# Optimization experiments

Measured on AMD Instinct MI355X. Metric: run time of the kernel, lower is better.

Reference implementation:

```python
import jax, jax.numpy as jnp
import numpy as np

B = 2048
NUM_ITER = 3  # dynamic routing iterations


def _conv2d(x, w, b, pad):
    # x: [B,C,H,W], w: [O,I,kh,kw] (OIHW)
    y = jax.lax.conv_general_dilated(
        x, w, window_strides=(1, 1), padding=[(pad, pad), (pad, pad)],
        dimension_numbers=('NCHW', 'OIHW', 'NCHW'))
    return y + b[None, :, None, None]


def _maxpool2(x):
    return jax.lax.reduce_window(x, -jnp.inf, jax.lax.max,
                                 (1, 1, 2, 2), (1, 1, 2, 2), 'VALID')


def _squash(t, axis=-1):
    # scale = |t|^2/(1+|t|^2); out = scale * t / |t|
    n2 = jnp.sum(t * t, axis=axis, keepdims=True)
    return (n2 / (1.0 + n2)) * t * jax.lax.rsqrt(n2)


def setup_inputs() -> dict:
    key = jax.random.key(0)
    ks = jax.random.split(key, 8)
    f32 = jnp.float32
    rn = lambda k, s, sc=1.0: jax.random.normal(k, s, f32) * sc
    return {
        'x': rn(ks[0], (B, 1, 36, 60)),
        'y': rn(ks[1], (B, 2)),
        'conv1_w': rn(ks[2], (20, 1, 5, 5), 0.1),
        'conv1_b': jnp.zeros((20,), f32),
        'conv2_w': rn(ks[3], (50, 20, 5, 5), 0.01),
        'conv2_b': jnp.zeros((50,), f32),
        'pcaps_w': rn(ks[4], (16, 50, 5, 5), 0.05),   # 4 capsules x 4 out-ch, stacked
        'pcaps_b': jnp.zeros((16,), f32),
        'route_w': rn(ks[5], (2, 288, 4, 1)),          # [num_caps, route_nodes, in_ch, out_ch]
        'fc1_w': rn(ks[6], (500, 3602), 0.02),
        'fc1_b': jnp.zeros((500,), f32),
        'fc2_w': rn(ks[7], (2, 502), 0.05),
        'fc2_b': jnp.zeros((2,), f32),
    }


def reference(x, y, conv1_w, conv1_b, conv2_w, conv2_b, pcaps_w, pcaps_b,
              route_w, fc1_w, fc1_b, fc2_w, fc2_b):
    b = x.shape[0]
    # conv backbone
    h = _maxpool2(_conv2d(x, conv1_w, conv1_b, 0))   # [B,20,16,28]
    h = _maxpool2(_conv2d(h, conv2_w, conv2_b, 0))   # [B,50,6,12]

    # primary capsules: 4 parallel convs (stacked into one), each [B,4,6,12]
    p = _conv2d(h, pcaps_w, pcaps_b, 2)              # [B,16,6,12]
    u = p.reshape(b, 4, 4 * 6 * 12)                  # [B, caps=4, nodes=288] (c,h,w flatten per capsule)
    u = u.transpose(0, 2, 1)                         # [B,288,4]
    u = _squash(u, axis=-1)

    # digit capsules: dynamic routing
    # priors[k,b,r,o] = sum_c u[b,r,c] * W[k,r,c,o]
    priors = jnp.einsum('brc,krco->kbro', u, route_w)  # [2,B,288,1]
    logits = jnp.zeros_like(priors)
    v = None
    for i in range(NUM_ITER):
        probs = jax.nn.softmax(logits, axis=2)
        v = _squash(jnp.sum(probs * priors, axis=2, keepdims=True), axis=-1)  # [2,B,1,1]
        if i < NUM_ITER - 1:
            logits = logits + jnp.sum(priors * v, axis=-1, keepdims=True)

    c = v[:, :, 0, :].transpose(1, 0, 2).reshape(b, -1)  # [B,2]
    xf = h.reshape(b, -1)                                # [B,3600]
    f = jnp.concatenate([xf, c], axis=-1)                # [B,3602]
    f = jax.nn.relu(f @ fc1_w.T + fc1_b)                 # [B,500]
    f = jnp.concatenate([f, y], axis=1)                  # [B,502]
    return f @ fc2_w.T + fc2_b                           # [B,2]
```

## Files before the change

kernel.cpp:

```cpp
#include <hip/hip_runtime.h>
#include <math.h>


#define BATCH 2048

typedef __attribute__((ext_vector_type(8))) short short8;
typedef __attribute__((ext_vector_type(4))) float floatx4;
typedef unsigned short u16;
typedef unsigned int   u32;

__device__ inline float wave_sum(float v) {
#pragma unroll
    for (int off = 32; off >= 1; off >>= 1) v += __shfl_xor(v, off);
    return v;
}
__device__ inline float wave_max(float v) {
#pragma unroll
    for (int off = 32; off >= 1; off >>= 1) v = fmaxf(v, __shfl_xor(v, off));
    return v;
}
__device__ inline u16 f2bf(float f) {
    u32 u = __float_as_uint(f);
    u32 r = (u + 0x7FFFu + ((u >> 16) & 1u)) >> 16;
    return (u16)r;
}

__global__ __launch_bounds__(256) void k_prep(
    const float* __restrict__ fw,  u16* __restrict__ w_bf,
    const float* __restrict__ w2,  u16* __restrict__ w2t,
    const float* __restrict__ pcw, u16* __restrict__ w_pc,
    const float* __restrict__ w1,  u16* __restrict__ w1t,
    const float* __restrict__ y,   const float* __restrict__ f2w,
    const float* __restrict__ f2b, float* __restrict__ out)
{
    __shared__ __align__(16) float srow[3600];
    const int blk = blockIdx.x, t = threadIdx.x;
    if (blk < 500) {
        const int n = blk;
        const float* src = fw + (size_t)n * 3602;
        for (int i = t; i < 1800; i += 256)
            *(float2*)&srow[2 * i] = *(const float2*)&src[2 * i];
        __syncthreads();
        u32* dst = (u32*)(w_bf + (size_t)n * 3616);
        for (int i = t; i < 1808; i += 256) {
            int k2 = 2 * i;
            u32 pk = 0u;
            if (k2 < 3600) {
                int pos = k2 / 50, oc = k2 - 50 * pos;
                pk = (u32)f2bf(srow[oc * 72 + pos])
                   | ((u32)f2bf(srow[(oc + 1) * 72 + pos]) << 16);
            }
            dst[i] = pk;
        }
    } else if (blk == 500) {
        u32* z = (u32*)(w_bf + (size_t)500 * 3616);
        for (int i = t; i < 21696; i += 256) z[i] = 0u;
    } else if (blk < 526) {
        int g   = (blk - 501) * 256 + t;
        int idx = g * 8;
        int tap = idx >> 11;
        int oc  = (idx >> 5) & 63;
        int ic0 = idx & 31;
        u16 v[8];
#pragma unroll
        for (int j = 0; j < 8; ++j) {
            int ic = ic0 + j;
            float f = (ic < 20 && oc < 50) ? w2[oc * 500 + ic * 25 + tap] : 0.f;
            v[j] = f2bf(f);
        }
        *(short8*)&w2t[idx] = *(short8*)v;
    } else if (blk < 539) {
        int g = (blk - 526) * 256 + t;
        if (g >= 3200) return;
        int idx = g * 8;
        int tap = idx >> 10;
        int rem = idx & 1023;
        int oc  = rem >> 6;
        int ic0 = rem & 63;
        u16 v[8];
#pragma unroll
        for (int j = 0; j < 8; ++j) {
            int ic = ic0 + j;
            float f = (ic < 50) ? pcw[(oc * 50 + ic) * 25 + tap] : 0.f;
            v[j] = f2bf(f);
        }
        *(short8*)&w_pc[idx] = *(short8*)v;
    } else if (blk == 539) {
        if (t < 128) {
            int n  = t >> 2;
            int k0 = (t & 3) * 8;
            u16 v[8];
#pragma unroll
            for (int j = 0; j < 8; ++j) {
                int k = k0 + j;
                float f = (n < 20 && k < 25) ? w1[n * 25 + k] : 0.f;
                v[j] = f2bf(f);
            }
            *(short8*)&w1t[t * 8] = *(short8*)v;
        }
    } else {
        int b = (blk - 540) * 256 + t;
        float y0 = y[b * 2], y1 = y[b * 2 + 1];
        float2 o;
        o.x = f2b[0] + y0 * f2w[500] + y1 * f2w[501];
        o.y = f2b[1] + y0 * f2w[502 + 500] + y1 * f2w[502 + 501];
        *(float2*)&out[b * 2] = o;
    }
}

__global__ __launch_bounds__(256, 3) void k_convs(
    const float* __restrict__ x, const u16* __restrict__ w1t,
    const float* __restrict__ b1, const u16* __restrict__ w2t,
    const float* __restrict__ b2, const u16* __restrict__ w_pc,
    const float* __restrict__ pcb, const float* __restrict__ rw,
    u32* __restrict__ h_bf, float* __restrict__ cbuf)
{
    __shared__ __align__(16) u16 smem[24704];
    u16* h1t = smem;
    u16* xbf = smem + 17920;
    u16* im2 = smem + 20224;

    const int t = threadIdx.x;
    const int b = blockIdx.x;

    for (int i = t; i < 2688; i += 256) {
        int pos = i / 6, c = i - 6 * pos;
        ((u32*)h1t)[pos * 20 + 10 + c] = 0u;
    }
    const float* xb = x + b * 2160;
    for (int i = t; i < 2160; i += 256) {
        int r = i / 60, c = i - 60 * r;
        xbf[r * 64 + c] = f2bf(xb[i]);
    }
    __syncthreads();

    const int lane = t & 63, w = t >> 6;
    const int r16  = lane & 15;
    const int q    = lane >> 4;

    short8 w1f[2];
#pragma unroll
    for (int nt = 0; nt < 2; ++nt)
        w1f[nt] = *(const short8*)&w1t[(nt * 16 + r16) * 32 + q * 8];

    const int p_   = t;
    const int px_  = p_ >> 2;
    const int dy_  = (p_ & 3) >> 1, dx_ = p_ & 1;
    const int xc_  = 2 * px_ + dx_;
    const int j0_  = xc_ >> 1;
    const int par_ = xc_ & 1;

#pragma unroll 1
    for (int c = 0; c < 16; ++c) {
        if (t < 112) {
            u16 tap[25];
#pragma unroll
            for (int r = 0; r < 5; ++r) {
                const u32* U = (const u32*)&xbf[(2 * c + dy_ + r) * 64];
                u32 A0 = U[j0_], A1 = U[j0_ + 1], A2 = U[j0_ + 2];
                u16 e0 = par_ ? (u16)(A0 >> 16) : (u16)A0;
                u16 e1 = par_ ? (u16)A1         : (u16)(A0 >> 16);
                u16 e2 = par_ ? (u16)(A1 >> 16) : (u16)A1;
                u16 e3 = par_ ? (u16)A2         : (u16)(A1 >> 16);
                u16 e4 = par_ ? (u16)(A2 >> 16) : (u16)A2;
                tap[r * 5 + 0] = e0; tap[r * 5 + 1] = e1; tap[r * 5 + 2] = e2;
                tap[r * 5 + 3] = e3; tap[r * 5 + 4] = e4;
            }
            u32 ow[16];
#pragma unroll
            for (int j = 0; j < 12; ++j)
                ow[j] = (u32)tap[2 * j] | ((u32)tap[2 * j + 1] << 16);
            ow[12] = (u32)tap[24];
            ow[13] = 0u; ow[14] = 0u; ow[15] = 0u;
            u32* dst = (u32*)&im2[p_ * 40];
            *(uint4*)&dst[0]  = make_uint4(ow[0],  ow[1],  ow[2],  ow[3]);
            *(uint4*)&dst[4]  = make_uint4(ow[4],  ow[5],  ow[6],  ow[7]);
            *(uint4*)&dst[8]  = make_uint4(ow[8],  ow[9],  ow[10], ow[11]);
            *(uint4*)&dst[12] = make_uint4(ow[12], ow[13], ow[14], ow[15]);
        }
        __syncthreads();
#pragma unroll
        for (int mi = 0; mi < 2; ++mi) {
            int mt = w + 4 * mi;
            if (mt < 7) {
                short8 af = *(const short8*)&im2[(mt * 16 + r16) * 40 + q * 8];
                floatx4 a1[2] = {};
#pragma unroll
                for (int nt = 0; nt < 2; ++nt)
                    a1[nt] = __builtin_amdgcn_mfma_f32_16x16x32_bf16(
                        af, w1f[nt], a1[nt], 0, 0, 0);
                int pq = mt * 4 + q;
#pragma unroll
                for (int nt = 0; nt < 2; ++nt) {
                    int oc = nt * 16 + r16;
                    if (oc < 20) {
                        floatx4 a = a1[nt];
                        float v = fmaxf(fmaxf(a[0], a[1]), fmaxf(a[2], a[3]))
                                + b1[oc];
                        h1t[(c * 28 + pq) * 40 + oc] = f2bf(v);
                    }
                }
            }
        }
        __syncthreads();
    }

    int abase[5];
#pragma unroll
    for (int i = 0; i < 5; ++i) {
        int mt = w + 4 * i;
        if (mt < 18) {
            int m  = mt * 16 + r16;
            int pq = m >> 2, sub = m & 3;
            int py = pq / 12, px = pq - py * 12;
            int yy = py * 2 + (sub >> 1);
            int xx = px * 2 + (sub & 1);
            abase[i] = (yy * 28 + xx) * 40 + q * 8;
        } else abase[i] = 0;
    }
    floatx4 acc2[5][4] = {};
    const u16* wtb = w2t + r16 * 32 + q * 8;

    short8 bf[4];
#pragma unroll
    for (int nt = 0; nt < 4; ++nt)
        bf[nt] = *(const short8*)&wtb[nt * 512];

#pragma unroll 1
    for (int tap = 0; tap < 25; ++tap) {
        short8 bfn[4];
        if (tap < 24) {
#pragma unroll
            for (int nt = 0; nt < 4; ++nt)
                bfn[nt] = *(const short8*)&wtb[(tap + 1) * 2048 + nt * 512];
        }
        int r = tap / 5, s = tap - 5 * r;
        int aoff = r * 1120 + s * 40;
#pragma unroll
        for (int i = 0; i < 5; ++i) {
            int mt = w + 4 * i;
            if (mt < 18) {
                short8 af = *(const short8*)&h1t[abase[i] + aoff];
#pragma unroll
                for (int nt = 0; nt < 4; ++nt)
                    acc2[i][nt] = __builtin_amdgcn_mfma_f32_16x16x32_bf16(
                        af, bf[nt], acc2[i][nt], 0, 0, 0);
            }
        }
#pragma unroll
        for (int nt = 0; nt < 4; ++nt) bf[nt] = bfn[nt];
    }
    __syncthreads();

    float* hs2 = (float*)smem;
#pragma unroll
    for (int i = 0; i < 5; ++i) {
        int mt = w + 4 * i;
        if (mt < 18) {
            int pq = mt * 4 + q;
#pragma unroll
            for (int nt = 0; nt < 4; ++nt) {
                int oc = nt * 16 + r16;
                if (oc < 50) {
                    floatx4 a = acc2[i][nt];
                    float v = fmaxf(fmaxf(a[0], a[1]), fmaxf(a[2], a[3])) + b2[oc];
                    hs2[pq * 50 + oc] = v;
                }
            }
        }
    }
    for (int i = t; i < 6336; i += 256)
        ((u32*)smem)[3600 + i] = 0u;
    __syncthreads();

    u16* hsbuf = smem + 7200;
    u32* ho = h_bf + (size_t)b * 1808;
    for (int i = t; i < 1808; i += 256) {
        if (i < 1800) {
            int k2 = 2 * i;
            u32 pk = (u32)f2bf(hs2[k2]) | ((u32)f2bf(hs2[k2 + 1]) << 16);
            ho[i] = pk;
            int pos = k2 / 50;
            int oc  = k2 - 50 * pos;
            int ph  = pos / 12, pw = pos - 12 * ph;
            ((u32*)hsbuf)[((((ph + 2) * 16) + pw + 2) * 72 + oc) >> 1] = pk;
        } else ho[i] = 0u;
    }
    __syncthreads();

    int pbase[5];
#pragma unroll
    for (int mt = 0; mt < 5; ++mt) {
        int m  = mt * 16 + r16;
        int ph = m / 12, pw = m - 12 * ph;
        pbase[mt] = (ph * 16 + pw) * 72 + q * 8;
    }
    floatx4 pacc[5] = {};
    const u16* wp = w_pc + r16 * 64 + q * 8;
    const int ntap = (28 - w) >> 2;
#pragma unroll 1
    for (int tt = 0; tt < ntap; ++tt) {
        int tap = w + 4 * tt;
        short8 b0 = *(const short8*)&wp[tap * 1024];
        short8 b1 = *(const short8*)&wp[tap * 1024 + 32];
        int r = tap / 5, s = tap - 5 * r;
        int aoff = (r * 16 + s) * 72;
#pragma unroll
        for (int mt = 0; mt < 5; ++mt) {
            short8 a0 = *(const short8*)&hsbuf[pbase[mt] + aoff];
            short8 a1 = *(const short8*)&hsbuf[pbase[mt] + aoff + 32];
            pacc[mt] = __builtin_amdgcn_mfma_f32_16x16x32_bf16(a0, b0, pacc[mt], 0, 0, 0);
            pacc[mt] = __builtin_amdgcn_mfma_f32_16x16x32_bf16(a1, b1, pacc[mt], 0, 0, 0);
        }
    }
    __syncthreads();

    float* psum = (float*)(smem + 7200);
#pragma unroll
    for (int mt = 0; mt < 5; ++mt)
#pragma unroll
        for (int i = 0; i < 4; ++i) {
            int m = mt * 16 + q * 4 + i;
            psum[w * 1280 + m * 16 + r16] = pacc[mt][i];
        }
    __syncthreads();

    for (int i = t; i < 1152; i += 256) {
        float s = psum[i] + psum[1280 + i] + psum[2560 + i] + psum[3840 + i]
                + pcb[i & 15];
        psum[i] = s;
    }
    __syncthreads();

    float* pri = (float*)(smem + 19872);
    for (int r = t; r < 288; r += 256) {
        int sub = r / 72;
        int pos = r - sub * 72;
        float u0 = psum[pos * 16 + 0  + sub];
        float u1 = psum[pos * 16 + 4  + sub];
        float u2 = psum[pos * 16 + 8  + sub];
        float u3 = psum[pos * 16 + 12 + sub];
        float n2 = u0 * u0 + u1 * u1 + u2 * u2 + u3 * u3;
        float scale = (n2 / (1.0f + n2)) * rsqrtf(n2);
        u0 *= scale; u1 *= scale; u2 *= scale; u3 *= scale;
#pragma unroll
        for (int k = 0; k < 2; ++k) {
            const float4 wv = *(const float4*)&rw[(k * 288 + r) * 4];
            pri[k * 288 + r] = u0 * wv.x + u1 * wv.y + u2 * wv.z + u3 * wv.w;
        }
    }
    __syncthreads();

    if (w < 2) {
        const float* pr = &pri[w * 288];
        float p[5];
        bool  val[5];
#pragma unroll
        for (int j = 0; j < 5; ++j) {
            int r  = j * 64 + lane;
            val[j] = r < 288;
            p[j]   = val[j] ? pr[r] : 0.0f;
        }
        float tot = wave_sum(p[0] + p[1] + p[2] + p[3] + p[4]);
        float s = tot * (1.0f / 288.0f);
        float a = s * fabsf(s) / (1.0f + s * s);
#pragma unroll
        for (int it = 0; it < 2; ++it) {
            float l[5];
            float lm = -INFINITY;
#pragma unroll
            for (int j = 0; j < 5; ++j) {
                l[j] = val[j] ? p[j] * a : -INFINITY;
                lm   = fmaxf(lm, l[j]);
            }
            lm = wave_max(lm);
            float se = 0.f, sp = 0.f;
#pragma unroll
            for (int j = 0; j < 5; ++j) {
                float e = val[j] ? expf(l[j] - lm) : 0.f;
                se += e;
                sp += e * p[j];
            }
            se = wave_sum(se);
            sp = wave_sum(sp);
            float sv = sp / se;
            float v  = sv * fabsf(sv) / (1.0f + sv * sv);
            if (it == 0) a += v;
            else if (lane == 0) cbuf[b * 2 + w] = v;
        }
    }
}

__global__ __launch_bounds__(256) void k_fc1(
    const u16* __restrict__ h_bf, const u16* __restrict__ w_bf,
    const float* __restrict__ cc, const float* __restrict__ w,
    const float* __restrict__ bias, const float* __restrict__ f2w,
    float* __restrict__ out)
{
    __shared__ __align__(16) u16 As[64 * 40];
    __shared__ __align__(16) u16 Bs[64 * 40];
    const int t  = threadIdx.x;
    const int m0 = blockIdx.x * 64;
    const int n0 = blockIdx.y * 64;
    const int row = t >> 2, c8 = (t & 3) * 8;
    const u16* ha = &h_bf[(size_t)(m0 + row) * 3616 + c8];
    const u16* wa = &w_bf[(size_t)(n0 + row) * 3616 + c8];
    short8 areg = *(const short8*)ha;
    short8 breg = *(const short8*)wa;
    const int lane = t & 63, wv = t >> 6;
    const int r16 = lane & 15, q = lane >> 4;
    const int wr = row * 40 + (t & 3) * 8;
    const int ar = (wv * 16 + r16) * 40 + q * 8;
    const int br = r16 * 40 + q * 8;
    floatx4 acc[4] = {};
#pragma unroll 1
    for (int it = 0; it < 113; ++it) {
        __syncthreads();
        *(short8*)&As[wr] = areg;
        *(short8*)&Bs[wr] = breg;
        __syncthreads();
        if (it < 112) {
            areg = *(const short8*)(ha + (it + 1) * 32);
            breg = *(const short8*)(wa + (it + 1) * 32);
        }
        short8 af = *(const short8*)&As[ar];
#pragma unroll
        for (int nt = 0; nt < 4; ++nt) {
            short8 bfv = *(const short8*)&Bs[nt * 640 + br];
            acc[nt] = __builtin_amdgcn_mfma_f32_16x16x32_bf16(af, bfv, acc[nt], 0, 0, 0);
        }
    }
    const int mbase = m0 + wv * 16 + q * 4;
    float s0[4] = {0.f, 0.f, 0.f, 0.f};
    float s1[4] = {0.f, 0.f, 0.f, 0.f};
#pragma unroll
    for (int nt = 0; nt < 4; ++nt) {
        int n = n0 + nt * 16 + r16;
        if (n < 500) {
            float bn  = bias[n];
            float wc0 = w[(size_t)n * 3602 + 3600];
            float wc1 = w[(size_t)n * 3602 + 3601];
            float w20 = f2w[n];
            float w21 = f2w[502 + n];
#pragma unroll
            for (int i = 0; i < 4; ++i) {
                int m = mbase + i;
                float v = fmaxf(acc[nt][i] + bn + cc[m * 2] * wc0
                                + cc[m * 2 + 1] * wc1, 0.f);
                s0[i] += v * w20;
                s1[i] += v * w21;
            }
        }
    }
#pragma unroll
    for (int i = 0; i < 4; ++i) {
        float a0 = s0[i], a1 = s1[i];
#pragma unroll
        for (int off = 1; off <= 8; off <<= 1) {
            a0 += __shfl_xor(a0, off);
            a1 += __shfl_xor(a1, off);
        }
        if (r16 == 0) {
            int m = mbase + i;
            atomicAdd(&out[m * 2], a0);
            atomicAdd(&out[m * 2 + 1], a1);
        }
    }
}

extern "C" void kernel_launch(void* const* d_in, const int* in_sizes, int n_in,
                              void* d_out, int out_size, void* d_ws, size_t ws_size,
                              hipStream_t stream) {
    const float* x    = (const float*)d_in[0];
    const float* y    = (const float*)d_in[1];
    const float* c1w  = (const float*)d_in[2];
    const float* c1b  = (const float*)d_in[3];
    const float* c2w  = (const float*)d_in[4];
    const float* c2b  = (const float*)d_in[5];
    const float* pcw  = (const float*)d_in[6];
    const float* pcb  = (const float*)d_in[7];
    const float* rw   = (const float*)d_in[8];
    const float* f1w  = (const float*)d_in[9];
    const float* f1b  = (const float*)d_in[10];
    const float* f2w  = (const float*)d_in[11];
    const float* f2b  = (const float*)d_in[12];
    float* out = (float*)d_out;

    u32*   h_bf = (u32*)d_ws;
    u16*   w_bf = (u16*)(h_bf + (size_t)BATCH * 1808);
    u16*   w2t  = w_bf + (size_t)512 * 3616;
    u16*   w_pc = w2t + 51200;
    u16*   w1t  = w_pc + 25600;
    float* cbuf = (float*)(w1t + 1024);

    k_prep<<<548, 256, 0, stream>>>(f1w, w_bf, c2w, w2t, pcw, w_pc, c1w, w1t,
                                    y, f2w, f2b, out);
    k_convs<<<BATCH, 256, 0, stream>>>(x, w1t, c1b, w2t, c2b, w_pc, pcb, rw,
                                       h_bf, cbuf);
    dim3 g4(32, 8);
    k_fc1<<<g4, 256, 0, stream>>>((const u16*)h_bf, w_bf, cbuf, f1w, f1b,
                                  f2w, out);
}
```

Baseline: 259.1 us.

## Build conv1 MFMA operands directly in registers, split conv2 accumulators, double-buffer fc1

Conv1 no longer stages an im2col tile in shared memory. Each lane now assembles its bf16 MFMA A-fragment straight from the input rows in registers, which removes the im2col buffer and the per-row barriers. Conv2 is split into two passes (3 tiles, then 2) to cut live accumulators, and the kernel asks for 4 blocks per CU instead of 3. fc1 moves to 32-row M tiles with double-buffered LDS and one barrier per step, doubling the grid. The cost is more register-side shuffling and redundant B-weight loads across the two conv2 passes.

```diff
diff --git a/kernel.cpp b/kernel.cpp
--- a/kernel.cpp
+++ b/kernel.cpp
@@ -23,6 +23,12 @@
     u32 u = __float_as_uint(f);
     u32 r = (u + 0x7FFFu + ((u >> 16) & 1u)) >> 16;
     return (u16)r;
+}
+__device__ inline void ext5(short8 v, int par, u16 e[5]) {
+    union { short8 s; u16 a[8]; } u; u.s = v;
+#pragma unroll
+    for (int s5 = 0; s5 < 5; ++s5)
+        e[s5] = par ? u.a[s5 + 1] : u.a[s5];
 }
 
 __global__ __launch_bounds__(256) void k_prep(
@@ -108,17 +114,16 @@
     }
 }
 
-__global__ __launch_bounds__(256, 3) void k_convs(
+__global__ __launch_bounds__(256, 4) void k_convs(
     const float* __restrict__ x, const u16* __restrict__ w1t,
     const float* __restrict__ b1, const u16* __restrict__ w2t,
     const float* __restrict__ b2, const u16* __restrict__ w_pc,
     const float* __restrict__ pcb, const float* __restrict__ rw,
     u32* __restrict__ h_bf, float* __restrict__ cbuf)
 {
-    __shared__ __align__(16) u16 smem[24704];
+    __shared__ __align__(16) u16 smem[20224];
     u16* h1t = smem;
     u16* xbf = smem + 17920;
-    u16* im2 = smem + 20224;
 
     const int t = threadIdx.x;
     const int b = blockIdx.x;
@@ -143,132 +148,181 @@
     for (int nt = 0; nt < 2; ++nt)
         w1f[nt] = *(const short8*)&w1t[(nt * 16 + r16) * 32 + q * 8];
 
-    const int p_   = t;
-    const int px_  = p_ >> 2;
-    const int dy_  = (p_ & 3) >> 1, dx_ = p_ & 1;
-    const int xc_  = 2 * px_ + dx_;
-    const int j0_  = xc_ >> 1;
-    const int par_ = xc_ & 1;
-
 #pragma unroll 1
-    for (int c = 0; c < 16; ++c) {
-        if (t < 112) {
-            u16 tap[25];
-#pragma unroll
-            for (int r = 0; r < 5; ++r) {
-                const u32* U = (const u32*)&xbf[(2 * c + dy_ + r) * 64];
-                u32 A0 = U[j0_], A1 = U[j0_ + 1], A2 = U[j0_ + 2];
-                u16 e0 = par_ ? (u16)(A0 >> 16) : (u16)A0;
-                u16 e1 = par_ ? (u16)A1         : (u16)(A0 >> 16);
-                u16 e2 = par_ ? (u16)(A1 >> 16) : (u16)A1;
-                u16 e3 = par_ ? (u16)A2         : (u16)(A1 >> 16);
-                u16 e4 = par_ ? (u16)(A2 >> 16) : (u16)A2;
-                tap[r * 5 + 0] = e0; tap[r * 5 + 1] = e1; tap[r * 5 + 2] = e2;
-                tap[r * 5 + 3] = e3; tap[r * 5 + 4] = e4;
-            }
-            u32 ow[16];
-#pragma unroll
-            for (int j = 0; j < 12; ++j)
-                ow[j] = (u32)tap[2 * j] | ((u32)tap[2 * j + 1] << 16);
-            ow[12] = (u32)tap[24];
-            ow[13] = 0u; ow[14] = 0u; ow[15] = 0u;
-            u32* dst = (u32*)&im2[p_ * 40];
-            *(uint4*)&dst[0]  = make_uint4(ow[0],  ow[1],  ow[2],  ow[3]);
-            *(uint4*)&dst[4]  = make_uint4(ow[4],  ow[5],  ow[6],  ow[7]);
-            *(uint4*)&dst[8]  = make_uint4(ow[8],  ow[9],  ow[10], ow[11]);
-            *(uint4*)&dst[12] = make_uint4(ow[12], ow[13], ow[14], ow[15]);
+    for (int jj = 0; jj < 28; ++jj) {
+        int jb = w + 4 * jj;
+        int mt = jb % 7;
+        int c  = jb / 7;
+        int p  = mt * 16 + r16;
+        int px = p >> 2;
+        int dy = (p >> 1) & 1, dx = p & 1;
+        int xc = 2 * px + dx;
+        int par = xc & 1;
+        int rowbase = (2 * c + dy) * 64 + (xc & ~1);
+        union { short8 s; u16 a[8]; } af;
+        if (q == 0) {
+            short8 vA = *(const short8*)&xbf[rowbase];
+            short8 vB = *(const short8*)&xbf[rowbase + 64];
+            u16 eA[5], eB[5];
+            ext5(vA, par, eA); ext5(vB, par, eB);
+            af.a[0]=eA[0]; af.a[1]=eA[1]; af.a[2]=eA[2]; af.a[3]=eA[3];
+            af.a[4]=eA[4]; af.a[5]=eB[0]; af.a[6]=eB[1]; af.a[7]=eB[2];
+        } else if (q == 1) {
+            short8 vB = *(const short8*)&xbf[rowbase + 64];
+            short8 vC = *(const short8*)&xbf[rowbase + 128];
+            short8 vD = *(const short8*)&xbf[rowbase + 192];
+            u16 eB[5], eC[5], eD[5];
+            ext5(vB, par, eB); ext5(vC, par, eC); ext5(vD, par, eD);
+            af.a[0]=eB[3]; af.a[1]=eB[4]; af.a[2]=eC[0]; af.a[3]=eC[1];
+            af.a[4]=eC[2]; af.a[5]=eC[3]; af.a[6]=eC[4]; af.a[7]=eD[0];
+        } else if (q == 2) {
+            short8 vD = *(const short8*)&xbf[rowbase + 192];
+            short8 vE = *(const short8*)&xbf[rowbase + 256];
+            u16 eD[5], eE[5];
+            ext5(vD, par, eD); ext5(vE, par, eE);
+            af.a[0]=eD[1]; af.a[1]=eD[2]; af.a[2]=eD[3]; af.a[3]=eD[4];
+            af.a[4]=eE[0]; af.a[5]=eE[1]; af.a[6]=eE[2]; af.a[7]=eE[3];
+        } else {
+            short8 vE = *(const short8*)&xbf[rowbase + 256];
+            u16 eE[5];
+            ext5(vE, par, eE);
+            af.a[0]=eE[4];
+#pragma unroll
+            for (int j = 1; j < 8; ++j) af.a[j] = 0;
+        }
+        floatx4 a1[2] = {};
+#pragma unroll
+        for (int nt = 0; nt < 2; ++nt)
+            a1[nt] = __builtin_amdgcn_mfma_f32_16x16x32_bf16(
+                af.s, w1f[nt], a1[nt], 0, 0, 0);
+        int pq = mt * 4 + q;
+#pragma unroll
+        for (int nt = 0; nt < 2; ++nt) {
+            int oc = nt * 16 + r16;
+            if (oc < 20) {
+                floatx4 a = a1[nt];
+                float v = fmaxf(fmaxf(a[0], a[1]), fmaxf(a[2], a[3])) + b1[oc];
+                h1t[(c * 28 + pq) * 40 + oc] = f2bf(v);
+            }
+        }
+    }
+    __syncthreads();
+
+    const u16* wtb = w2t + r16 * 32 + q * 8;
+    float* hs2 = (float*)smem;
+
+    {
+        int abase[3];
+#pragma unroll
+        for (int i = 0; i < 3; ++i) {
+            int m  = (w + 4 * i) * 16 + r16;
+            int pq = m >> 2, sub = m & 3;
+            int py = pq / 12, px2 = pq - py * 12;
+            int yy = py * 2 + (sub >> 1);
+            int xx = px2 * 2 + (sub & 1);
+            abase[i] = (yy * 28 + xx) * 40 + q * 8;
+        }
+        floatx4 acc[3][4] = {};
+        short8 bf[4];
+#pragma unroll
+        for (int nt = 0; nt < 4; ++nt)
+            bf[nt] = *(const short8*)&wtb[nt * 512];
+#pragma unroll 1
+        for (int tap = 0; tap < 25; ++tap) {
+            short8 bfn[4];
+            if (tap < 24) {
+#pragma unroll
+                for (int nt = 0; nt < 4; ++nt)
+                    bfn[nt] = *(const short8*)&wtb[(tap + 1) * 2048 + nt * 512];
+            }
+            int r = tap / 5, s = tap - 5 * r;
+            int aoff = r * 1120 + s * 40;
+#pragma unroll
+            for (int i = 0; i < 3; ++i) {
+                short8 af = *(const short8*)&h1t[abase[i] + aoff];
+#pragma unroll
+                for (int nt = 0; nt < 4; ++nt)
+                    acc[i][nt] = __builtin_amdgcn_mfma_f32_16x16x32_bf16(
+                        af, bf[nt], acc[i][nt], 0, 0, 0);
+            }
+#pragma unroll
+            for (int nt = 0; nt < 4; ++nt) bf[nt] = bfn[nt];
         }
         __syncthreads();
 #pragma unroll
-        for (int mi = 0; mi < 2; ++mi) {
-            int mt = w + 4 * mi;
-            if (mt < 7) {
-                short8 af = *(const short8*)&im2[(mt * 16 + r16) * 40 + q * 8];
-                floatx4 a1[2] = {};
-#pragma unroll
-                for (int nt = 0; nt < 2; ++nt)
-                    a1[nt] = __builtin_amdgcn_mfma_f32_16x16x32_bf16(
-                        af, w1f[nt], a1[nt], 0, 0, 0);
-                int pq = mt * 4 + q;
-#pragma unroll
-                for (int nt = 0; nt < 2; ++nt) {
-                    int oc = nt * 16 + r16;
-                    if (oc < 20) {
-                        floatx4 a = a1[nt];
-                        float v = fmaxf(fmaxf(a[0], a[1]), fmaxf(a[2], a[3]))
-                                + b1[oc];
-                        h1t[(c * 28 + pq) * 40 + oc] = f2bf(v);
-                    }
-                }
-            }
-        }
-        __syncthreads();
-    }
-
-    int abase[5];
-#pragma unroll
-    for (int i = 0; i < 5; ++i) {
-        int mt = w + 4 * i;
-        if (mt < 18) {
-            int m  = mt * 16 + r16;
-            int pq = m >> 2, sub = m & 3;
-            int py = pq / 12, px = pq - py * 12;
-            int yy = py * 2 + (sub >> 1);
-            int xx = px * 2 + (sub & 1);
-            abase[i] = (yy * 28 + xx) * 40 + q * 8;
-        } else abase[i] = 0;
-    }
-    floatx4 acc2[5][4] = {};
-    const u16* wtb = w2t + r16 * 32 + q * 8;
-
-    short8 bf[4];
-#pragma unroll
-    for (int nt = 0; nt < 4; ++nt)
-        bf[nt] = *(const short8*)&wtb[nt * 512];
-
-#pragma unroll 1
-    for (int tap = 0; tap < 25; ++tap) {
-        short8 bfn[4];
-        if (tap < 24) {
-#pragma unroll
-            for (int nt = 0; nt < 4; ++nt)
-                bfn[nt] = *(const short8*)&wtb[(tap + 1) * 2048 + nt * 512];
-        }
-        int r = tap / 5, s = tap - 5 * r;
-        int aoff = r * 1120 + s * 40;
-#pragma unroll
-        for (int i = 0; i < 5; ++i) {
-            int mt = w + 4 * i;
-            if (mt < 18) {
-                short8 af = *(const short8*)&h1t[abase[i] + aoff];
-#pragma unroll
-                for (int nt = 0; nt < 4; ++nt)
-                    acc2[i][nt] = __builtin_amdgcn_mfma_f32_16x16x32_bf16(
-                        af, bf[nt], acc2[i][nt], 0, 0, 0);
-            }
-        }
-#pragma unroll
-        for (int nt = 0; nt < 4; ++nt) bf[nt] = bfn[nt];
-    }
-    __syncthreads();
-
-    float* hs2 = (float*)smem;
-#pragma unroll
-    for (int i = 0; i < 5; ++i) {
-        int mt = w + 4 * i;
-        if (mt < 18) {
-            int pq = mt * 4 + q;
+        for (int i = 0; i < 3; ++i) {
+            int pq = (w + 4 * i) * 4 + q;
 #pragma unroll
             for (int nt = 0; nt < 4; ++nt) {
                 int oc = nt * 16 + r16;
                 if (oc < 50) {
-                    floatx4 a = acc2[i][nt];
-                    float v = fmaxf(fmaxf(a[0], a[1]), fmaxf(a[2], a[3])) + b2[oc];
-                    hs2[pq * 50 + oc] = v;
+                    floatx4 a = acc[i][nt];
+                    hs2[pq * 50 + oc] =
+                        fmaxf(fmaxf(a[0], a[1]), fmaxf(a[2], a[3])) + b2[oc];
                 }
             }
         }
     }
+    {
+        int abase[2];
+        bool vld[2];
+#pragma unroll
+        for (int i = 0; i < 2; ++i) {
+            int mt = w + 12 + 4 * i;
+            vld[i] = (mt < 18);
+            int m  = (vld[i] ? mt : 12) * 16 + r16;
+            int pq = m >> 2, sub = m & 3;
+            int py = pq / 12, px2 = pq - py * 12;
+            int yy = py * 2 + (sub >> 1);
+            int xx = px2 * 2 + (sub & 1);
+            abase[i] = (yy * 28 + xx) * 40 + q * 8;
+        }
+        floatx4 acc[2][4] = {};
+        short8 bf[4];
+#pragma unroll
+        for (int nt = 0; nt < 4; ++nt)
+            bf[nt] = *(const short8*)&wtb[nt * 512];
+#pragma unroll 1
+        for (int tap = 0; tap < 25; ++tap) {
+            short8 bfn[4];
+            if (tap < 24) {
+#pragma unroll
+                for (int nt = 0; nt < 4; ++nt)
+                    bfn[nt] = *(const short8*)&wtb[(tap + 1) * 2048 + nt * 512];
+            }
+            int r = tap / 5, s = tap - 5 * r;
+            int aoff = r * 1120 + s * 40;
+#pragma unroll
+            for (int i = 0; i < 2; ++i) {
+                if (vld[i]) {
+                    short8 af = *(const short8*)&h1t[abase[i] + aoff];
+#pragma unroll
+                    for (int nt = 0; nt < 4; ++nt)
+                        acc[i][nt] = __builtin_amdgcn_mfma_f32_16x16x32_bf16(
+                            af, bf[nt], acc[i][nt], 0, 0, 0);
+                }
+            }
+#pragma unroll
+            for (int nt = 0; nt < 4; ++nt) bf[nt] = bfn[nt];
+        }
+#pragma unroll
+        for (int i = 0; i < 2; ++i) {
+            if (vld[i]) {
+                int pq = (w + 12 + 4 * i) * 4 + q;
+#pragma unroll
+                for (int nt = 0; nt < 4; ++nt) {
+                    int oc = nt * 16 + r16;
+                    if (oc < 50) {
+                        floatx4 a = acc[i][nt];
+                        hs2[pq * 50 + oc] =
+                            fmaxf(fmaxf(a[0], a[1]), fmaxf(a[2], a[3])) + b2[oc];
+                    }
+                }
+            }
+        }
+    }
+    __syncthreads();
+
     for (int i = t; i < 6336; i += 256)
         ((u32*)smem)[3600 + i] = 0u;
     __syncthreads();
@@ -332,7 +386,7 @@
     }
     __syncthreads();
 
-    float* pri = (float*)(smem + 19872);
+    float* pri = (float*)(smem + 17440);
     for (int r = t; r < 288; r += 256) {
         int sub = r / 72;
         int pos = r - sub * 72;
@@ -397,45 +451,50 @@
     const float* __restrict__ bias, const float* __restrict__ f2w,
     float* __restrict__ out)
 {
-    __shared__ __align__(16) u16 As[64 * 40];
-    __shared__ __align__(16) u16 Bs[64 * 40];
+    __shared__ __align__(16) u16 As[2][32 * 40];
+    __shared__ __align__(16) u16 Bs[2][64 * 40];
     const int t  = threadIdx.x;
-    const int m0 = blockIdx.x * 64;
+    const int m0 = blockIdx.x * 32;
     const int n0 = blockIdx.y * 64;
-    const int row = t >> 2, c8 = (t & 3) * 8;
-    const u16* ha = &h_bf[(size_t)(m0 + row) * 3616 + c8];
-    const u16* wa = &w_bf[(size_t)(n0 + row) * 3616 + c8];
-    short8 areg = *(const short8*)ha;
-    short8 breg = *(const short8*)wa;
     const int lane = t & 63, wv = t >> 6;
     const int r16 = lane & 15, q = lane >> 4;
-    const int wr = row * 40 + (t & 3) * 8;
-    const int ar = (wv * 16 + r16) * 40 + q * 8;
-    const int br = r16 * 40 + q * 8;
-    floatx4 acc[4] = {};
+    const int row = t >> 2, c8 = (t & 3) * 8;
+    const bool aload = (t < 128);
+    const u16* ha = &h_bf[(size_t)(m0 + (row & 31)) * 3616 + c8];
+    const u16* wa = &w_bf[(size_t)(n0 + row) * 3616 + c8];
+    short8 areg = {};
+    if (aload) areg = *(const short8*)ha;
+    short8 breg = *(const short8*)wa;
+    const int mt  = wv & 1;
+    const int ntb = (wv >> 1) * 2;
+    const int awr = (row & 31) * 40 + c8;
+    const int bwr = row * 40 + c8;
+    const int ar  = (mt * 16 + r16) * 40 + q * 8;
+    const int br0 = (ntb * 16 + r16) * 40 + q * 8;
+    floatx4 acc[2] = {};
 #pragma unroll 1
     for (int it = 0; it < 113; ++it) {
+        const int buf = it & 1;
+        if (aload) *(short8*)&As[buf][awr] = areg;
+        *(short8*)&Bs[buf][bwr] = breg;
+        if (it < 112) {
+            if (aload) areg = *(const short8*)(ha + (it + 1) * 32);
+            breg = *(const short8*)(wa + (it + 1) * 32);
+        }
         __syncthreads();
-        *(short8*)&As[wr] = areg;
-        *(short8*)&Bs[wr] = breg;
-        __syncthreads();
-        if (it < 112) {
-            areg = *(const short8*)(ha + (it + 1) * 32);
-            breg = *(const short8*)(wa + (it + 1) * 32);
-        }
-        short8 af = *(const short8*)&As[ar];
-#pragma unroll
-        for (int nt = 0; nt < 4; ++nt) {
-            short8 bfv = *(const short8*)&Bs[nt * 640 + br];
-            acc[nt] = __builtin_amdgcn_mfma_f32_16x16x32_bf16(af, bfv, acc[nt], 0, 0, 0);
-        }
-    }
-    const int mbase = m0 + wv * 16 + q * 4;
+        short8 af = *(const short8*)&As[buf][ar];
+#pragma unroll
+        for (int jn = 0; jn < 2; ++jn) {
+            short8 bfv = *(const short8*)&Bs[buf][br0 + jn * 640];
+            acc[jn] = __builtin_amdgcn_mfma_f32_16x16x32_bf16(af, bfv, acc[jn], 0, 0, 0);
+        }
+    }
+    const int mbase = m0 + mt * 16 + q * 4;
     float s0[4] = {0.f, 0.f, 0.f, 0.f};
     float s1[4] = {0.f, 0.f, 0.f, 0.f};
 #pragma unroll
-    for (int nt = 0; nt < 4; ++nt) {
-        int n = n0 + nt * 16 + r16;
+    for (int jn = 0; jn < 2; ++jn) {
+        int n = n0 + (ntb + jn) * 16 + r16;
         if (n < 500) {
             float bn  = bias[n];
             float wc0 = w[(size_t)n * 3602 + 3600];
@@ -445,7 +504,7 @@
 #pragma unroll
             for (int i = 0; i < 4; ++i) {
                 int m = mbase + i;
-                float v = fmaxf(acc[nt][i] + bn + cc[m * 2] * wc0
+                float v = fmaxf(acc[jn][i] + bn + cc[m * 2] * wc0
                                 + cc[m * 2 + 1] * wc1, 0.f);
                 s0[i] += v * w20;
                 s1[i] += v * w21;
@@ -497,7 +556,7 @@
                                     y, f2w, f2b, out);
     k_convs<<<BATCH, 256, 0, stream>>>(x, w1t, c1b, w2t, c2b, w_pc, pcb, rw,
                                        h_bf, cbuf);
-    dim3 g4(32, 8);
+    dim3 g4(64, 8);
     k_fc1<<<g4, 256, 0, stream>>>((const u16*)h_bf, w_bf, cbuf, f1w, f1b,
                                   f2w, out);
 }
```

Result: slower. 283.5 us (+9.4%).

## Double-buffer fc1 LDS tiles and double the K step per iteration

Applied to the files above, without the earlier changes.

The fc1 GEMM kernel now keeps two LDS buffers and loads a 64-wide K slice per iteration instead of 32. This cuts the barriers to one per iteration and halves the iteration count. The padded K stride grows from 3616 to 3648 so it is a multiple of 64, which means updating the weight prep, the activation writes and the workspace offsets to match. In exchange the kernel uses more LDS and more registers for the prefetch, and the extra zero padding adds a little memory traffic.

```diff
diff --git a/kernel.cpp b/kernel.cpp
--- a/kernel.cpp
+++ b/kernel.cpp
@@ -3,6 +3,7 @@
 
 
 #define BATCH 2048
+#define KP 3648
 
 typedef __attribute__((ext_vector_type(8))) short short8;
 typedef __attribute__((ext_vector_type(4))) float floatx4;
@@ -41,8 +42,8 @@
         for (int i = t; i < 1800; i += 256)
             *(float2*)&srow[2 * i] = *(const float2*)&src[2 * i];
         __syncthreads();
-        u32* dst = (u32*)(w_bf + (size_t)n * 3616);
-        for (int i = t; i < 1808; i += 256) {
+        u32* dst = (u32*)(w_bf + (size_t)n * KP);
+        for (int i = t; i < 1824; i += 256) {
             int k2 = 2 * i;
             u32 pk = 0u;
             if (k2 < 3600) {
@@ -53,8 +54,8 @@
             dst[i] = pk;
         }
     } else if (blk == 500) {
-        u32* z = (u32*)(w_bf + (size_t)500 * 3616);
-        for (int i = t; i < 21696; i += 256) z[i] = 0u;
+        u32* z = (u32*)(w_bf + (size_t)500 * KP);
+        for (int i = t; i < 21888; i += 256) z[i] = 0u;
     } else if (blk < 526) {
         int g   = (blk - 501) * 256 + t;
         int idx = g * 8;
@@ -263,8 +264,8 @@
                 int oc = nt * 16 + r16;
                 if (oc < 50) {
                     floatx4 a = acc2[i][nt];
-                    float v = fmaxf(fmaxf(a[0], a[1]), fmaxf(a[2], a[3])) + b2[oc];
-                    hs2[pq * 50 + oc] = v;
+                    hs2[pq * 50 + oc] =
+                        fmaxf(fmaxf(a[0], a[1]), fmaxf(a[2], a[3])) + b2[oc];
                 }
             }
         }
@@ -274,8 +275,8 @@
     __syncthreads();
 
     u16* hsbuf = smem + 7200;
-    u32* ho = h_bf + (size_t)b * 1808;
-    for (int i = t; i < 1808; i += 256) {
+    u32* ho = h_bf + (size_t)b * 1824;
+    for (int i = t; i < 1824; i += 256) {
         if (i < 1800) {
             int k2 = 2 * i;
             u32 pk = (u32)f2bf(hs2[k2]) | ((u32)f2bf(hs2[k2 + 1]) << 16);
@@ -397,37 +398,49 @@
     const float* __restrict__ bias, const float* __restrict__ f2w,
     float* __restrict__ out)
 {
-    __shared__ __align__(16) u16 As[64 * 40];
-    __shared__ __align__(16) u16 Bs[64 * 40];
+    __shared__ __align__(16) u16 As[2][64 * 72];
+    __shared__ __align__(16) u16 Bs[2][64 * 72];
     const int t  = threadIdx.x;
     const int m0 = blockIdx.x * 64;
     const int n0 = blockIdx.y * 64;
-    const int row = t >> 2, c8 = (t & 3) * 8;
-    const u16* ha = &h_bf[(size_t)(m0 + row) * 3616 + c8];
-    const u16* wa = &w_bf[(size_t)(n0 + row) * 3616 + c8];
-    short8 areg = *(const short8*)ha;
-    short8 breg = *(const short8*)wa;
+    const int row = t >> 2, seg = t & 3;
+    const u16* ha = &h_bf[(size_t)(m0 + row) * KP + seg * 16];
+    const u16* wa = &w_bf[(size_t)(n0 + row) * KP + seg * 16];
+    short8 a0 = *(const short8*)ha;
+    short8 a1 = *(const short8*)(ha + 8);
+    short8 b0 = *(const short8*)wa;
+    short8 b1 = *(const short8*)(wa + 8);
     const int lane = t & 63, wv = t >> 6;
     const int r16 = lane & 15, q = lane >> 4;
-    const int wr = row * 40 + (t & 3) * 8;
-    const int ar = (wv * 16 + r16) * 40 + q * 8;
-    const int br = r16 * 40 + q * 8;
+    const int wr = row * 72 + seg * 16;
+    const int ar = (wv * 16 + r16) * 72 + q * 8;
+    const int br = r16 * 72 + q * 8;
     floatx4 acc[4] = {};
 #pragma unroll 1
-    for (int it = 0; it < 113; ++it) {
+    for (int it = 0; it < 57; ++it) {
+        const int buf = it & 1;
+        *(short8*)&As[buf][wr]     = a0;
+        *(short8*)&As[buf][wr + 8] = a1;
+        *(short8*)&Bs[buf][wr]     = b0;
+        *(short8*)&Bs[buf][wr + 8] = b1;
+        if (it < 56) {
+            const u16* han = ha + (it + 1) * 64;
+            const u16* wan = wa + (it + 1) * 64;
+            a0 = *(const short8*)han;
+            a1 = *(const short8*)(han + 8);
+            b0 = *(const short8*)wan;
+            b1 = *(const short8*)(wan + 8);
+        }
         __syncthreads();
-        *(short8*)&As[wr] = areg;
-        *(short8*)&Bs[wr] = breg;
-        __syncthreads();
-        if (it < 112) {
-            areg = *(const short8*)(ha + (it + 1) * 32);
-            breg = *(const short8*)(wa + (it + 1) * 32);
-        }
-        short8 af = *(const short8*)&As[ar];
-#pragma unroll
-        for (int nt = 0; nt < 4; ++nt) {
-            short8 bfv = *(const short8*)&Bs[nt * 640 + br];
-            acc[nt] = __builtin_amdgcn_mfma_f32_16x16x32_bf16(af, bfv, acc[nt], 0, 0, 0);
+#pragma unroll
+        for (int s = 0; s < 2; ++s) {
+            short8 af = *(const short8*)&As[buf][ar + s * 32];
+#pragma unroll
+            for (int nt = 0; nt < 4; ++nt) {
+                short8 bfv = *(const short8*)&Bs[buf][br + nt * 1152 + s * 32];
+                acc[nt] = __builtin_amdgcn_mfma_f32_16x16x32_bf16(
+                    af, bfv, acc[nt], 0, 0, 0);
+            }
         }
     }
     const int mbase = m0 + wv * 16 + q * 4;
@@ -454,16 +467,16 @@
     }
 #pragma unroll
     for (int i = 0; i < 4; ++i) {
-        float a0 = s0[i], a1 = s1[i];
+        float a0r = s0[i], a1r = s1[i];
 #pragma unroll
         for (int off = 1; off <= 8; off <<= 1) {
-            a0 += __shfl_xor(a0, off);
-            a1 += __shfl_xor(a1, off);
+            a0r += __shfl_xor(a0r, off);
+            a1r += __shfl_xor(a1r, off);
         }
         if (r16 == 0) {
             int m = mbase + i;
-            atomicAdd(&out[m * 2], a0);
-            atomicAdd(&out[m * 2 + 1], a1);
+            atomicAdd(&out[m * 2], a0r);
+            atomicAdd(&out[m * 2 + 1], a1r);
         }
     }
 }
@@ -487,8 +500,8 @@
     float* out = (float*)d_out;
 
     u32*   h_bf = (u32*)d_ws;
-    u16*   w_bf = (u16*)(h_bf + (size_t)BATCH * 1808);
-    u16*   w2t  = w_bf + (size_t)512 * 3616;
+    u16*   w_bf = (u16*)(h_bf + (size_t)BATCH * 1824);
+    u16*   w2t  = w_bf + (size_t)512 * KP;
     u16*   w_pc = w2t + 51200;
     u16*   w1t  = w_pc + 25600;
     float* cbuf = (float*)(w1t + 1024);
```

New measurement: 237.2 us. 8.4% less time.

## Split-K FC1 with global_load_lds tiles and separate FC2 reduction kernel

Applied to the files above, without the earlier changes.

The FC1 GEMM is restructured into a split-K kernel (4 K-slices, 128x64 tiles) that loads tiles directly into LDS via global_load_lds, and writes partial sums to a workspace. A new k_fc2 kernel then sums the partials, applies bias, capsule terms and ReLU, and computes the FC2 outputs without atomics, using a precomputed per-neuron weight table. K padding grows to 3712 to divide evenly, and the psum LDS layout is padded to stride 17 to avoid bank conflicts. This aims to raise parallelism and memory throughput in FC1, at the cost of an extra launch and a large fp32 partial-sum buffer round trip.

```diff
diff --git a/kernel.cpp b/kernel.cpp
--- a/kernel.cpp
+++ b/kernel.cpp
@@ -3,11 +3,16 @@
 
 
 #define BATCH 2048
+#define KP 3712
 
 typedef __attribute__((ext_vector_type(8))) short short8;
 typedef __attribute__((ext_vector_type(4))) float floatx4;
 typedef unsigned short u16;
 typedef unsigned int   u32;
+
+#define GLD(gp, lp) __builtin_amdgcn_global_load_lds( \
+    (const __attribute__((address_space(1))) u32*)(gp), \
+    (__attribute__((address_space(3))) u32*)(lp), 16, 0, 0)
 
 __device__ inline float wave_sum(float v) {
 #pragma unroll
@@ -30,8 +35,8 @@
     const float* __restrict__ w2,  u16* __restrict__ w2t,
     const float* __restrict__ pcw, u16* __restrict__ w_pc,
     const float* __restrict__ w1,  u16* __restrict__ w1t,
-    const float* __restrict__ y,   const float* __restrict__ f2w,
-    const float* __restrict__ f2b, float* __restrict__ out)
+    const float* __restrict__ f1b, const float* __restrict__ f2w,
+    float* __restrict__ wtab)
 {
     __shared__ __align__(16) float srow[3600];
     const int blk = blockIdx.x, t = threadIdx.x;
@@ -41,8 +46,8 @@
         for (int i = t; i < 1800; i += 256)
             *(float2*)&srow[2 * i] = *(const float2*)&src[2 * i];
         __syncthreads();
-        u32* dst = (u32*)(w_bf + (size_t)n * 3616);
-        for (int i = t; i < 1808; i += 256) {
+        u32* dst = (u32*)(w_bf + (size_t)n * KP);
+        for (int i = t; i < 1856; i += 256) {
             int k2 = 2 * i;
             u32 pk = 0u;
             if (k2 < 3600) {
@@ -53,8 +58,8 @@
             dst[i] = pk;
         }
     } else if (blk == 500) {
-        u32* z = (u32*)(w_bf + (size_t)500 * 3616);
-        for (int i = t; i < 21696; i += 256) z[i] = 0u;
+        u32* z = (u32*)(w_bf + (size_t)500 * KP);
+        for (int i = t; i < 22272; i += 256) z[i] = 0u;
     } else if (blk < 526) {
         int g   = (blk - 501) * 256 + t;
         int idx = g * 8;
@@ -99,12 +104,18 @@
             *(short8*)&w1t[t * 8] = *(short8*)v;
         }
     } else {
-        int b = (blk - 540) * 256 + t;
-        float y0 = y[b * 2], y1 = y[b * 2 + 1];
-        float2 o;
-        o.x = f2b[0] + y0 * f2w[500] + y1 * f2w[501];
-        o.y = f2b[1] + y0 * f2w[502 + 500] + y1 * f2w[502 + 501];
-        *(float2*)&out[b * 2] = o;
+        for (int nn = t; nn < 512; nn += 256) {
+            float bias = 0.f, wc0 = 0.f, wc1 = 0.f, f20 = 0.f, f21 = 0.f;
+            if (nn < 500) {
+                bias = f1b[nn];
+                wc0  = fw[(size_t)nn * 3602 + 3600];
+                wc1  = fw[(size_t)nn * 3602 + 3601];
+                f20  = f2w[nn];
+                f21  = f2w[502 + nn];
+            }
+            *(float4*)&wtab[nn * 8]     = make_float4(bias, wc0, wc1, f20);
+            *(float4*)&wtab[nn * 8 + 4] = make_float4(f21, 0.f, 0.f, 0.f);
+        }
     }
 }
 
@@ -263,8 +274,8 @@
                 int oc = nt * 16 + r16;
                 if (oc < 50) {
                     floatx4 a = acc2[i][nt];
-                    float v = fmaxf(fmaxf(a[0], a[1]), fmaxf(a[2], a[3])) + b2[oc];
-                    hs2[pq * 50 + oc] = v;
+                    hs2[pq * 50 + oc] =
+                        fmaxf(fmaxf(a[0], a[1]), fmaxf(a[2], a[3])) + b2[oc];
                 }
             }
         }
@@ -274,8 +285,8 @@
     __syncthreads();
 
     u16* hsbuf = smem + 7200;
-    u32* ho = h_bf + (size_t)b * 1808;
-    for (int i = t; i < 1808; i += 256) {
+    u32* ho = h_bf + (size_t)b * 1856;
+    for (int i = t; i < 1856; i += 256) {
         if (i < 1800) {
             int k2 = 2 * i;
             u32 pk = (u32)f2bf(hs2[k2]) | ((u32)f2bf(hs2[k2 + 1]) << 16);
@@ -321,14 +332,16 @@
 #pragma unroll
         for (int i = 0; i < 4; ++i) {
             int m = mt * 16 + q * 4 + i;
-            psum[w * 1280 + m * 16 + r16] = pacc[mt][i];
+            psum[w * 1360 + m * 17 + r16] = pacc[mt][i];
         }
     __syncthreads();
 
     for (int i = t; i < 1152; i += 256) {
-        float s = psum[i] + psum[1280 + i] + psum[2560 + i] + psum[3840 + i]
-                + pcb[i & 15];
-        psum[i] = s;
+        int m = i >> 4, oc = i & 15;
+        int a = m * 17 + oc;
+        float s = psum[a] + psum[1360 + a] + psum[2720 + a] + psum[4080 + a]
+                + pcb[oc];
+        psum[a] = s;
     }
     __syncthreads();
 
@@ -336,10 +349,10 @@
     for (int r = t; r < 288; r += 256) {
         int sub = r / 72;
         int pos = r - sub * 72;
-        float u0 = psum[pos * 16 + 0  + sub];
-        float u1 = psum[pos * 16 + 4  + sub];
-        float u2 = psum[pos * 16 + 8  + sub];
-        float u3 = psum[pos * 16 + 12 + sub];
+        float u0 = psum[pos * 17 + 0  + sub];
+        float u1 = psum[pos * 17 + 4  + sub];
+        float u2 = psum[pos * 17 + 8  + sub];
+        float u3 = psum[pos * 17 + 12 + sub];
         float n2 = u0 * u0 + u1 * u1 + u2 * u2 + u3 * u3;
         float scale = (n2 / (1.0f + n2)) * rsqrtf(n2);
         u0 *= scale; u1 *= scale; u2 *= scale; u3 *= scale;
@@ -393,78 +406,92 @@
 
 __global__ __launch_bounds__(256) void k_fc1(
     const u16* __restrict__ h_bf, const u16* __restrict__ w_bf,
-    const float* __restrict__ cc, const float* __restrict__ w,
-    const float* __restrict__ bias, const float* __restrict__ f2w,
+    float* __restrict__ f1buf)
+{
+    __shared__ __align__(16) u16 As[128 * 32];
+    __shared__ __align__(16) u16 Bs[64 * 32];
+    const int t = threadIdx.x;
+    const int lane = t & 63, w = t >> 6;
+    const int m0 = blockIdx.x * 128;
+    const int n0 = blockIdx.y * 64;
+    const int s  = blockIdx.z;
+    const int k0 = s * 928;
+
+    const int ai0 = (w * 2) * 64 + lane;
+    const int ai1 = (w * 2 + 1) * 64 + lane;
+    const int bi  = w * 64 + lane;
+    const u16* ga0 = h_bf + (size_t)(m0 + (ai0 >> 2)) * KP + k0 + (ai0 & 3) * 8;
+    const u16* ga1 = h_bf + (size_t)(m0 + (ai1 >> 2)) * KP + k0 + (ai1 & 3) * 8;
+    const u16* gb  = w_bf + (size_t)(n0 + (bi  >> 2)) * KP + k0 + (bi  & 3) * 8;
+    u16* lA0 = As + (w * 2) * 512;
+    u16* lA1 = As + (w * 2 + 1) * 512;
+    u16* lB  = Bs + w * 512;
+
+    const int r16 = lane & 15, q = lane >> 4;
+    const int ar = (w * 32 + r16) * 32 + q * 8;
+    const int br = r16 * 32 + q * 8;
+
+    floatx4 acc[2][4] = {};
+#pragma unroll 1
+    for (int it = 0; it < 29; ++it) {
+        const int ko = it * 32;
+        GLD(ga0 + ko, lA0);
+        GLD(ga1 + ko, lA1);
+        GLD(gb + ko, lB);
+        __syncthreads();
+        short8 af0 = *(const short8*)&As[ar];
+        short8 af1 = *(const short8*)&As[ar + 512];
+#pragma unroll
+        for (int nt = 0; nt < 4; ++nt) {
+            short8 bfv = *(const short8*)&Bs[br + nt * 512];
+            acc[0][nt] = __builtin_amdgcn_mfma_f32_16x16x32_bf16(af0, bfv, acc[0][nt], 0, 0, 0);
+            acc[1][nt] = __builtin_amdgcn_mfma_f32_16x16x32_bf16(af1, bfv, acc[1][nt], 0, 0, 0);
+        }
+        __syncthreads();
+    }
+
+    float* fo = f1buf + (size_t)s * (2048 * 512);
+    const int mb = m0 + w * 32;
+#pragma unroll
+    for (int mt2 = 0; mt2 < 2; ++mt2)
+#pragma unroll
+        for (int nt = 0; nt < 4; ++nt) {
+            int n = n0 + nt * 16 + r16;
+#pragma unroll
+            for (int i = 0; i < 4; ++i) {
+                int m = mb + mt2 * 16 + q * 4 + i;
+                fo[(size_t)m * 512 + n] = acc[mt2][nt][i];
+            }
+        }
+}
+
+__global__ __launch_bounds__(256) void k_fc2(
+    const float* __restrict__ f1buf, const float* __restrict__ wtab,
+    const float* __restrict__ cc, const float* __restrict__ y,
+    const float* __restrict__ f2w, const float* __restrict__ f2b,
     float* __restrict__ out)
 {
-    __shared__ __align__(16) u16 As[64 * 40];
-    __shared__ __align__(16) u16 Bs[64 * 40];
-    const int t  = threadIdx.x;
-    const int m0 = blockIdx.x * 64;
-    const int n0 = blockIdx.y * 64;
-    const int row = t >> 2, c8 = (t & 3) * 8;
-    const u16* ha = &h_bf[(size_t)(m0 + row) * 3616 + c8];
-    const u16* wa = &w_bf[(size_t)(n0 + row) * 3616 + c8];
-    short8 areg = *(const short8*)ha;
-    short8 breg = *(const short8*)wa;
-    const int lane = t & 63, wv = t >> 6;
-    const int r16 = lane & 15, q = lane >> 4;
-    const int wr = row * 40 + (t & 3) * 8;
-    const int ar = (wv * 16 + r16) * 40 + q * 8;
-    const int br = r16 * 40 + q * 8;
-    floatx4 acc[4] = {};
-#pragma unroll 1
-    for (int it = 0; it < 113; ++it) {
-        __syncthreads();
-        *(short8*)&As[wr] = areg;
-        *(short8*)&Bs[wr] = breg;
-        __syncthreads();
-        if (it < 112) {
-            areg = *(const short8*)(ha + (it + 1) * 32);
-            breg = *(const short8*)(wa + (it + 1) * 32);
-        }
-        short8 af = *(const short8*)&As[ar];
-#pragma unroll
-        for (int nt = 0; nt < 4; ++nt) {
-            short8 bfv = *(const short8*)&Bs[nt * 640 + br];
-            acc[nt] = __builtin_amdgcn_mfma_f32_16x16x32_bf16(af, bfv, acc[nt], 0, 0, 0);
-        }
-    }
-    const int mbase = m0 + wv * 16 + q * 4;
-    float s0[4] = {0.f, 0.f, 0.f, 0.f};
-    float s1[4] = {0.f, 0.f, 0.f, 0.f};
-#pragma unroll
-    for (int nt = 0; nt < 4; ++nt) {
-        int n = n0 + nt * 16 + r16;
-        if (n < 500) {
-            float bn  = bias[n];
-            float wc0 = w[(size_t)n * 3602 + 3600];
-            float wc1 = w[(size_t)n * 3602 + 3601];
-            float w20 = f2w[n];
-            float w21 = f2w[502 + n];
-#pragma unroll
-            for (int i = 0; i < 4; ++i) {
-                int m = mbase + i;
-                float v = fmaxf(acc[nt][i] + bn + cc[m * 2] * wc0
-                                + cc[m * 2 + 1] * wc1, 0.f);
-                s0[i] += v * w20;
-                s1[i] += v * w21;
-            }
-        }
-    }
-#pragma unroll
-    for (int i = 0; i < 4; ++i) {
-        float a0 = s0[i], a1 = s1[i];
-#pragma unroll
-        for (int off = 1; off <= 8; off <<= 1) {
-            a0 += __shfl_xor(a0, off);
-            a1 += __shfl_xor(a1, off);
-        }
-        if (r16 == 0) {
-            int m = mbase + i;
-            atomicAdd(&out[m * 2], a0);
-            atomicAdd(&out[m * 2 + 1], a1);
-        }
+    const int b = blockIdx.x * 4 + (threadIdx.x >> 6);
+    const int lane = threadIdx.x & 63;
+    const float* fb = f1buf + (size_t)b * 512;
+    const float c0 = cc[b * 2], c1 = cc[b * 2 + 1];
+    float s0 = 0.f, s1 = 0.f;
+#pragma unroll
+    for (int j = 0; j < 8; ++j) {
+        int n = lane + j * 64;
+        float raw = fb[n] + fb[1048576 + n] + fb[2097152 + n] + fb[3145728 + n];
+        float4 t0 = *(const float4*)&wtab[n * 8];
+        float  f21 = wtab[n * 8 + 4];
+        float v = fmaxf(raw + t0.x + c0 * t0.y + c1 * t0.z, 0.f);
+        s0 += v * t0.w;
+        s1 += v * f21;
+    }
+    s0 = wave_sum(s0);
+    s1 = wave_sum(s1);
+    if (lane == 0) {
+        float y0 = y[b * 2], y1 = y[b * 2 + 1];
+        out[b * 2]     = s0 + f2b[0] + y0 * f2w[500] + y1 * f2w[501];
+        out[b * 2 + 1] = s1 + f2b[1] + y0 * f2w[1002] + y1 * f2w[1003];
     }
 }
 
@@ -486,18 +513,20 @@
     const float* f2b  = (const float*)d_in[12];
     float* out = (float*)d_out;
 
-    u32*   h_bf = (u32*)d_ws;
-    u16*   w_bf = (u16*)(h_bf + (size_t)BATCH * 1808);
-    u16*   w2t  = w_bf + (size_t)512 * 3616;
-    u16*   w_pc = w2t + 51200;
-    u16*   w1t  = w_pc + 25600;
-    float* cbuf = (float*)(w1t + 1024);
-
-    k_prep<<<548, 256, 0, stream>>>(f1w, w_bf, c2w, w2t, pcw, w_pc, c1w, w1t,
-                                    y, f2w, f2b, out);
+    u32*   h_bf  = (u32*)d_ws;
+    u16*   w_bf  = (u16*)(h_bf + (size_t)BATCH * 1856);
+    u16*   w2t   = w_bf + (size_t)512 * KP;
+    u16*   w_pc  = w2t + 51200;
+    u16*   w1t   = w_pc + 25600;
+    float* cbuf  = (float*)(w1t + 1024);
+    float* wtab  = cbuf + 4096;
+    float* f1buf = wtab + 4096;
+
+    k_prep<<<541, 256, 0, stream>>>(f1w, w_bf, c2w, w2t, pcw, w_pc, c1w, w1t,
+                                    f1b, f2w, wtab);
     k_convs<<<BATCH, 256, 0, stream>>>(x, w1t, c1b, w2t, c2b, w_pc, pcb, rw,
                                        h_bf, cbuf);
-    dim3 g4(32, 8);
-    k_fc1<<<g4, 256, 0, stream>>>((const u16*)h_bf, w_bf, cbuf, f1w, f1b,
-                                  f2w, out);
-}
+    dim3 g4(16, 8, 4);
+    k_fc1<<<g4, 256, 0, stream>>>((const u16*)h_bf, w_bf, f1buf);
+    k_fc2<<<BATCH / 4, 256, 0, stream>>>(f1buf, wtab, cbuf, y, f2w, f2b, out);
+}
```

Measured after the change: 236.6 us. 1.09x faster.
